# Performance work log

Hardware: AMD Instinct MI355X
Metric: run time of the kernel (lower is better)

The kernel has to match this reference:

```python
import jax, jax.numpy as jnp
import numpy as np

N_ROWS = 8388608          # multiple of 4, as required by the chunked linear
N_SEGMENTS = 4096


def setup_inputs() -> dict:
    key = jax.random.key(0)
    kx, ks = jax.random.split(key)
    x = jax.random.normal(kx, (N_ROWS, 4), dtype=jnp.float32)
    # monotone segment boundaries: 0 = slices[0] <= ... <= slices[-1] = N_ROWS
    interior = jnp.sort(jax.random.randint(ks, (N_SEGMENTS - 1,), 1, N_ROWS, dtype=jnp.int32))
    slices = jnp.concatenate([jnp.zeros((1,), jnp.int32), interior,
                              jnp.full((1,), N_ROWS, jnp.int32)])
    # fixed weight from the original module: arange(16).reshape(4, 4)
    W = jnp.arange(16, dtype=jnp.float32).reshape(4, 4)
    return {"x": x, "slices": slices, "W": W}


def reference(x, slices, W):
    # Chunked 4-row linear == plain matmul with the same weight (nn.Linear: y = x @ W.T)
    y = x @ W.T                                           # [N, 4]
    n = y.shape[0]
    # segment id of each row: number of boundaries <= row index, minus 1
    seg = jnp.searchsorted(slices, jnp.arange(n, dtype=slices.dtype), side="right") - 1
    seg = jnp.clip(seg, 0, N_SEGMENTS - 1)
    # per-segment sum of |y| over all elements (rows and features)
    seg_abs = jax.ops.segment_sum(jnp.abs(y).sum(-1), seg, num_segments=N_SEGMENTS)  # [S]
    return y / seg_abs[seg][:, None]
```

## Files before the change

### kernel.cpp

```cpp
#include <hip/hip_runtime.h>


#define NSEG  4096
#define BLK   256
#define RPT   32
#define BATCH 8
#define CHUNK (BLK * RPT)
#define WSZ   64

typedef float v4 __attribute__((ext_vector_type(4)));

__device__ __forceinline__ float absrow(v4 v, const float* w) {
    float y0 = fabsf(v.x * w[0]  + v.y * w[1]  + v.z * w[2]  + v.w * w[3]);
    float y1 = fabsf(v.x * w[4]  + v.y * w[5]  + v.z * w[6]  + v.w * w[7]);
    float y2 = fabsf(v.x * w[8]  + v.y * w[9]  + v.z * w[10] + v.w * w[11]);
    float y3 = fabsf(v.x * w[12] + v.y * w[13] + v.z * w[14] + v.w * w[15]);
    return (y0 + y1) + (y2 + y3);
}

__device__ __forceinline__ void flush_seg(float acc, int seg, int s0,
                                          float* hist, float* __restrict__ seg_abs) {
    if (acc == 0.0f) return;
    int d = seg - s0;
    if (d < WSZ) atomicAdd(&hist[d], acc);
    else         atomicAdd(&seg_abs[seg], acc);
}

__global__ __launch_bounds__(BLK) void seg_pass1(
    const v4* __restrict__ x, const int* __restrict__ slices,
    const float* __restrict__ W, float* __restrict__ seg_abs, int n)
{
    __shared__ float hist[WSZ];
    __shared__ int s0_sh;
    if (threadIdx.x < WSZ) hist[threadIdx.x] = 0.0f;

    float w[16];
#pragma unroll
    for (int i = 0; i < 16; ++i) w[i] = W[i];

    const int base = blockIdx.x * CHUNK + threadIdx.x;

    int r0 = (base < n) ? base : (n - 1);
    int lo = 0, hi = NSEG;
    while (hi - lo > 1) { int mid = (lo + hi) >> 1; if (slices[mid] <= r0) lo = mid; else hi = mid; }
    int seg = lo;
    if (threadIdx.x == 0) s0_sh = seg;
    __syncthreads();
    const int s0 = s0_sh;

    int   nextb = slices[seg + 1];
    float acc   = 0.0f;

    const bool full = (base + (RPT - 1) * BLK) < n;
    if (full) {
#pragma unroll
        for (int b = 0; b < RPT / BATCH; ++b) {
            v4 d[BATCH];
#pragma unroll
            for (int j = 0; j < BATCH; ++j)
                d[j] = x[base + (b * BATCH + j) * BLK];
#pragma unroll
            for (int j = 0; j < BATCH; ++j) {
                int r = base + (b * BATCH + j) * BLK;
                if (r >= nextb) {
                    flush_seg(acc, seg, s0, hist, seg_abs);
                    acc = 0.0f;
                    do { ++seg; nextb = slices[seg + 1]; } while (r >= nextb);
                }
                acc += absrow(d[j], w);
            }
        }
    } else {
        for (int it = 0; it < RPT; ++it) {
            int r = base + it * BLK;
            if (r < n) {
                if (r >= nextb) {
                    flush_seg(acc, seg, s0, hist, seg_abs);
                    acc = 0.0f;
                    do { ++seg; nextb = slices[seg + 1]; } while (r >= nextb);
                }
                acc += absrow(x[r], w);
            }
        }
    }
    flush_seg(acc, seg, s0, hist, seg_abs);
    __syncthreads();

    if (threadIdx.x < WSZ) {
        float h = hist[threadIdx.x];
        if (h != 0.0f) atomicAdd(&seg_abs[s0 + threadIdx.x], h);
    }
}

__global__ __launch_bounds__(BLK) void seg_pass2(
    const v4* __restrict__ x, const int* __restrict__ slices,
    const float* __restrict__ W, const float* __restrict__ seg_abs,
    v4* __restrict__ out, int n)
{
    float w[16];
#pragma unroll
    for (int i = 0; i < 16; ++i) w[i] = W[i];

    const int base = blockIdx.x * CHUNK + threadIdx.x;

    int r0 = (base < n) ? base : (n - 1);
    int lo = 0, hi = NSEG;
    while (hi - lo > 1) { int mid = (lo + hi) >> 1; if (slices[mid] <= r0) lo = mid; else hi = mid; }
    int seg = lo;

    int   nextb = slices[seg + 1];
    float inv   = 1.0f / seg_abs[seg];

    const bool full = (base + (RPT - 1) * BLK) < n;
    if (full) {
#pragma unroll
        for (int b = 0; b < RPT / BATCH; ++b) {
            v4 d[BATCH];
#pragma unroll
            for (int j = 0; j < BATCH; ++j)
                d[j] = x[base + (b * BATCH + j) * BLK];
#pragma unroll
            for (int j = 0; j < BATCH; ++j) {
                int r = base + (b * BATCH + j) * BLK;
                if (r >= nextb) {
                    do { ++seg; nextb = slices[seg + 1]; } while (r >= nextb);
                    inv = 1.0f / seg_abs[seg];
                }
                v4 v = d[j], o;
                o.x = (v.x * w[0]  + v.y * w[1]  + v.z * w[2]  + v.w * w[3])  * inv;
                o.y = (v.x * w[4]  + v.y * w[5]  + v.z * w[6]  + v.w * w[7])  * inv;
                o.z = (v.x * w[8]  + v.y * w[9]  + v.z * w[10] + v.w * w[11]) * inv;
                o.w = (v.x * w[12] + v.y * w[13] + v.z * w[14] + v.w * w[15]) * inv;
                __builtin_nontemporal_store(o, &out[r]);
            }
        }
    } else {
        for (int it = 0; it < RPT; ++it) {
            int r = base + it * BLK;
            if (r < n) {
                if (r >= nextb) {
                    do { ++seg; nextb = slices[seg + 1]; } while (r >= nextb);
                    inv = 1.0f / seg_abs[seg];
                }
                v4 v = x[r], o;
                o.x = (v.x * w[0]  + v.y * w[1]  + v.z * w[2]  + v.w * w[3])  * inv;
                o.y = (v.x * w[4]  + v.y * w[5]  + v.z * w[6]  + v.w * w[7])  * inv;
                o.z = (v.x * w[8]  + v.y * w[9]  + v.z * w[10] + v.w * w[11]) * inv;
                o.w = (v.x * w[12] + v.y * w[13] + v.z * w[14] + v.w * w[15]) * inv;
                __builtin_nontemporal_store(o, &out[r]);
            }
        }
    }
}

extern "C" void kernel_launch(void* const* d_in, const int* in_sizes, int n_in,
                              void* d_out, int out_size, void* d_ws, size_t ws_size,
                              hipStream_t stream) {
    const v4*    x       = (const v4*)d_in[0];
    const int*   slices  = (const int*)d_in[1];
    const float* W       = (const float*)d_in[2];
    float*       seg_abs = (float*)d_ws;
    v4*          out     = (v4*)d_out;
    int n = in_sizes[0] / 4;

    hipMemsetAsync(d_ws, 0, NSEG * sizeof(float), stream);

    int nblocks = (n + CHUNK - 1) / CHUNK;
    seg_pass1<<<nblocks, BLK, 0, stream>>>(x, slices, W, seg_abs, n);
    seg_pass2<<<nblocks, BLK, 0, stream>>>(x, slices, W, seg_abs, out, n);
}
```

Measured before the change: 261.1 us.

## Fuse segment-sum and normalize into one kernel with redundant per-block segment reduction

Replaces the memset plus two-pass scheme with a single kernel in which each block recomputes the full |y| sums for every segment overlapping its chunk, reading rows outside its chunk as needed, and then normalizes its own rows from shared memory. This removes the global atomics, the memset and the second launch, and the chunk's own rows are likely still in cache when they are read back. The cost is redundant reads of long boundary segments (up to about a million rows each, so on average several times the chunk size per block), which makes total traffic grow considerably. It also remaps block ids across the 8 XCDs so neighbouring chunks share an L2, and adds a per-row fallback for chunks that span 256 or more segments.

```diff
diff --git a/kernel.cpp b/kernel.cpp
--- a/kernel.cpp
+++ b/kernel.cpp
@@ -4,9 +4,9 @@
 #define NSEG  4096
 #define BLK   256
 #define RPT   32
-#define BATCH 8
 #define CHUNK (BLK * RPT)
-#define WSZ   64
+#define WSZ   256
+#define NXCD  8
 
 typedef float v4 __attribute__((ext_vector_type(4)));
 
@@ -18,154 +18,146 @@
     return (y0 + y1) + (y2 + y3);
 }
 
-__device__ __forceinline__ void flush_seg(float acc, int seg, int s0,
-                                          float* hist, float* __restrict__ seg_abs) {
-    if (acc == 0.0f) return;
-    int d = seg - s0;
-    if (d < WSZ) atomicAdd(&hist[d], acc);
-    else         atomicAdd(&seg_abs[seg], acc);
-}
-
-__global__ __launch_bounds__(BLK) void seg_pass1(
+__global__ __launch_bounds__(BLK) void seg_norm_fused(
     const v4* __restrict__ x, const int* __restrict__ slices,
-    const float* __restrict__ W, float* __restrict__ seg_abs, int n)
+    const float* __restrict__ W, v4* __restrict__ out, int n, int nblocks)
 {
     __shared__ float hist[WSZ];
-    __shared__ int s0_sh;
-    if (threadIdx.x < WSZ) hist[threadIdx.x] = 0.0f;
+    hist[threadIdx.x] = 0.0f;
 
     float w[16];
 #pragma unroll
     for (int i = 0; i < 16; ++i) w[i] = W[i];
 
-    const int base = blockIdx.x * CHUNK + threadIdx.x;
+    int c = blockIdx.x;
+    if ((nblocks & (NXCD - 1)) == 0) {
+        int per = nblocks / NXCD;
+        c = (int)(blockIdx.x & (NXCD - 1)) * per + (int)(blockIdx.x / NXCD);
+    }
 
-    int r0 = (base < n) ? base : (n - 1);
-    int lo = 0, hi = NSEG;
-    while (hi - lo > 1) { int mid = (lo + hi) >> 1; if (slices[mid] <= r0) lo = mid; else hi = mid; }
-    int seg = lo;
-    if (threadIdx.x == 0) s0_sh = seg;
+    const int cs = c * CHUNK;
+    const int ce = (cs + CHUNK < n) ? (cs + CHUNK) : n;
+
+    int s_first, s_last;
+    {
+        int lo = 0, hi = NSEG;
+        while (hi - lo > 1) { int m = (lo + hi) >> 1; if (slices[m] <= cs) lo = m; else hi = m; }
+        s_first = lo;
+        lo = 0; hi = NSEG;
+        const int rl = ce - 1;
+        while (hi - lo > 1) { int m = (lo + hi) >> 1; if (slices[m] <= rl) lo = m; else hi = m; }
+        s_last = lo;
+    }
+
+    if (s_last - s_first >= WSZ) {
+        for (int r = cs + (int)threadIdx.x; r < ce; r += BLK) {
+            int lo = 0, hi = NSEG;
+            while (hi - lo > 1) { int m = (lo + hi) >> 1; if (slices[m] <= r) lo = m; else hi = m; }
+            float ssum = 0.0f;
+            const int b0 = slices[lo], b1 = slices[lo + 1];
+            for (int q = b0; q < b1; ++q) ssum += absrow(x[q], w);
+            const float inv = 1.0f / ssum;
+            v4 v = x[r], o;
+            o.x = (v.x * w[0]  + v.y * w[1]  + v.z * w[2]  + v.w * w[3])  * inv;
+            o.y = (v.x * w[4]  + v.y * w[5]  + v.z * w[6]  + v.w * w[7])  * inv;
+            o.z = (v.x * w[8]  + v.y * w[9]  + v.z * w[10] + v.w * w[11]) * inv;
+            o.w = (v.x * w[12] + v.y * w[13] + v.z * w[14] + v.w * w[15]) * inv;
+            __builtin_nontemporal_store(o, &out[r]);
+        }
+        return;
+    }
+
     __syncthreads();
-    const int s0 = s0_sh;
 
+    const int R0 = slices[s_first];
+    const int R1 = slices[s_last + 1];
+
+    int   seg   = s_first;
     int   nextb = slices[seg + 1];
     float acc   = 0.0f;
 
-    const bool full = (base + (RPT - 1) * BLK) < n;
-    if (full) {
+    int r = R0 + (int)threadIdx.x;
+    for (; r + 7 * BLK < R1; r += 8 * BLK) {
+        v4 d[8];
 #pragma unroll
-        for (int b = 0; b < RPT / BATCH; ++b) {
-            v4 d[BATCH];
+        for (int j = 0; j < 8; ++j)
+            d[j] = x[r + j * BLK];
 #pragma unroll
-            for (int j = 0; j < BATCH; ++j)
-                d[j] = x[base + (b * BATCH + j) * BLK];
-#pragma unroll
-            for (int j = 0; j < BATCH; ++j) {
-                int r = base + (b * BATCH + j) * BLK;
-                if (r >= nextb) {
-                    flush_seg(acc, seg, s0, hist, seg_abs);
-                    acc = 0.0f;
-                    do { ++seg; nextb = slices[seg + 1]; } while (r >= nextb);
-                }
-                acc += absrow(d[j], w);
+        for (int j = 0; j < 8; ++j) {
+            const int rr = r + j * BLK;
+            if (rr >= nextb) {
+                if (acc != 0.0f) atomicAdd(&hist[seg - s_first], acc);
+                acc = 0.0f;
+                do { ++seg; nextb = slices[seg + 1]; } while (rr >= nextb);
             }
-        }
-    } else {
-        for (int it = 0; it < RPT; ++it) {
-            int r = base + it * BLK;
-            if (r < n) {
-                if (r >= nextb) {
-                    flush_seg(acc, seg, s0, hist, seg_abs);
-                    acc = 0.0f;
-                    do { ++seg; nextb = slices[seg + 1]; } while (r >= nextb);
-                }
-                acc += absrow(x[r], w);
-            }
+            acc += absrow(d[j], w);
         }
     }
-    flush_seg(acc, seg, s0, hist, seg_abs);
+    for (; r < R1; r += BLK) {
+        if (r >= nextb) {
+            if (acc != 0.0f) atomicAdd(&hist[seg - s_first], acc);
+            acc = 0.0f;
+            do { ++seg; nextb = slices[seg + 1]; } while (r >= nextb);
+        }
+        acc += absrow(x[r], w);
+    }
+    if (acc != 0.0f) atomicAdd(&hist[seg - s_first], acc);
+
+    __syncthreads();
+    {
+        const float h = hist[threadIdx.x];
+        hist[threadIdx.x] = (h > 0.0f) ? (1.0f / h) : 0.0f;
+    }
     __syncthreads();
 
-    if (threadIdx.x < WSZ) {
-        float h = hist[threadIdx.x];
-        if (h != 0.0f) atomicAdd(&seg_abs[s0 + threadIdx.x], h);
+    seg   = s_first;
+    nextb = slices[seg + 1];
+    float inv = hist[0];
+
+    r = cs + (int)threadIdx.x;
+    for (; r + 7 * BLK < ce; r += 8 * BLK) {
+        v4 d[8];
+#pragma unroll
+        for (int j = 0; j < 8; ++j)
+            d[j] = x[r + j * BLK];
+#pragma unroll
+        for (int j = 0; j < 8; ++j) {
+            const int rr = r + j * BLK;
+            if (rr >= nextb) {
+                do { ++seg; nextb = slices[seg + 1]; } while (rr >= nextb);
+                inv = hist[seg - s_first];
+            }
+            v4 v = d[j], o;
+            o.x = (v.x * w[0]  + v.y * w[1]  + v.z * w[2]  + v.w * w[3])  * inv;
+            o.y = (v.x * w[4]  + v.y * w[5]  + v.z * w[6]  + v.w * w[7])  * inv;
+            o.z = (v.x * w[8]  + v.y * w[9]  + v.z * w[10] + v.w * w[11]) * inv;
+            o.w = (v.x * w[12] + v.y * w[13] + v.z * w[14] + v.w * w[15]) * inv;
+            __builtin_nontemporal_store(o, &out[rr]);
+        }
     }
-}
-
-__global__ __launch_bounds__(BLK) void seg_pass2(
-    const v4* __restrict__ x, const int* __restrict__ slices,
-    const float* __restrict__ W, const float* __restrict__ seg_abs,
-    v4* __restrict__ out, int n)
-{
-    float w[16];
-#pragma unroll
-    for (int i = 0; i < 16; ++i) w[i] = W[i];
-
-    const int base = blockIdx.x * CHUNK + threadIdx.x;
-
-    int r0 = (base < n) ? base : (n - 1);
-    int lo = 0, hi = NSEG;
-    while (hi - lo > 1) { int mid = (lo + hi) >> 1; if (slices[mid] <= r0) lo = mid; else hi = mid; }
-    int seg = lo;
-
-    int   nextb = slices[seg + 1];
-    float inv   = 1.0f / seg_abs[seg];
-
-    const bool full = (base + (RPT - 1) * BLK) < n;
-    if (full) {
-#pragma unroll
-        for (int b = 0; b < RPT / BATCH; ++b) {
-            v4 d[BATCH];
-#pragma unroll
-            for (int j = 0; j < BATCH; ++j)
-                d[j] = x[base + (b * BATCH + j) * BLK];
-#pragma unroll
-            for (int j = 0; j < BATCH; ++j) {
-                int r = base + (b * BATCH + j) * BLK;
-                if (r >= nextb) {
-                    do { ++seg; nextb = slices[seg + 1]; } while (r >= nextb);
-                    inv = 1.0f / seg_abs[seg];
-                }
-                v4 v = d[j], o;
-                o.x = (v.x * w[0]  + v.y * w[1]  + v.z * w[2]  + v.w * w[3])  * inv;
-                o.y = (v.x * w[4]  + v.y * w[5]  + v.z * w[6]  + v.w * w[7])  * inv;
-                o.z = (v.x * w[8]  + v.y * w[9]  + v.z * w[10] + v.w * w[11]) * inv;
-                o.w = (v.x * w[12] + v.y * w[13] + v.z * w[14] + v.w * w[15]) * inv;
-                __builtin_nontemporal_store(o, &out[r]);
-            }
+    for (; r < ce; r += BLK) {
+        if (r >= nextb) {
+            do { ++seg; nextb = slices[seg + 1]; } while (r >= nextb);
+            inv = hist[seg - s_first];
         }
-    } else {
-        for (int it = 0; it < RPT; ++it) {
-            int r = base + it * BLK;
-            if (r < n) {
-                if (r >= nextb) {
-                    do { ++seg; nextb = slices[seg + 1]; } while (r >= nextb);
-                    inv = 1.0f / seg_abs[seg];
-                }
-                v4 v = x[r], o;
-                o.x = (v.x * w[0]  + v.y * w[1]  + v.z * w[2]  + v.w * w[3])  * inv;
-                o.y = (v.x * w[4]  + v.y * w[5]  + v.z * w[6]  + v.w * w[7])  * inv;
-                o.z = (v.x * w[8]  + v.y * w[9]  + v.z * w[10] + v.w * w[11]) * inv;
-                o.w = (v.x * w[12] + v.y * w[13] + v.z * w[14] + v.w * w[15]) * inv;
-                __builtin_nontemporal_store(o, &out[r]);
-            }
-        }
+        v4 v = x[r], o;
+        o.x = (v.x * w[0]  + v.y * w[1]  + v.z * w[2]  + v.w * w[3])  * inv;
+        o.y = (v.x * w[4]  + v.y * w[5]  + v.z * w[6]  + v.w * w[7])  * inv;
+        o.z = (v.x * w[8]  + v.y * w[9]  + v.z * w[10] + v.w * w[11]) * inv;
+        o.w = (v.x * w[12] + v.y * w[13] + v.z * w[14] + v.w * w[15]) * inv;
+        __builtin_nontemporal_store(o, &out[r]);
     }
 }
 
 extern "C" void kernel_launch(void* const* d_in, const int* in_sizes, int n_in,
                               void* d_out, int out_size, void* d_ws, size_t ws_size,
                               hipStream_t stream) {
-    const v4*    x       = (const v4*)d_in[0];
-    const int*   slices  = (const int*)d_in[1];
-    const float* W       = (const float*)d_in[2];
-    float*       seg_abs = (float*)d_ws;
-    v4*          out     = (v4*)d_out;
+    const v4*    x      = (const v4*)d_in[0];
+    const int*   slices = (const int*)d_in[1];
+    const float* W      = (const float*)d_in[2];
+    v4*          out    = (v4*)d_out;
     int n = in_sizes[0] / 4;
+    int nblocks = (n + CHUNK - 1) / CHUNK;
 
-    hipMemsetAsync(d_ws, 0, NSEG * sizeof(float), stream);
-
-    int nblocks = (n + CHUNK - 1) / CHUNK;
-    seg_pass1<<<nblocks, BLK, 0, stream>>>(x, slices, W, seg_abs, n);
-    seg_pass2<<<nblocks, BLK, 0, stream>>>(x, slices, W, seg_abs, out, n);
+    seg_norm_fused<<<nblocks, BLK, 0, stream>>>(x, slices, W, out, n, nblocks);
 }
```

Result: no change. 259.4 us (-0.6%).
